# Optimization experiments

Measured on AMD Instinct MI355X. Metric: run time of the kernel, lower is better.

## Reference

```python
import jax, jax.numpy as jnp
import numpy as np

B, C, H, W = 8, 3, 1024, 1024
N, D, PS, NB, NH = 512, 256, 16, 8, 4


def _bin_matrix():
    # static radial-binning averaging matrix for a PS x (PS//2+1) rfft2 spectrum
    h, w = PS, PS // 2 + 1
    fy = np.fft.fftfreq(h)
    fx = np.linspace(0.0, 0.5, w)
    r = np.sqrt(fx[None, :] ** 2 + fy[:, None] ** 2)
    max_r = r.max() + 1e-6
    edges = np.linspace(0.0, max_r, NB + 1)
    idx = np.clip(np.searchsorted(edges, r.ravel(), side='right') - 1, 0, NB - 1)
    M = np.zeros((NB, h * w), np.float32)
    M[idx, np.arange(h * w)] = 1.0
    cnt = M.sum(1, keepdims=True)
    return M / np.maximum(cnt, 1.0)

_BIN_M = jnp.asarray(_bin_matrix())


def _ln(x, g, b, eps=1e-5):
    m = x.mean(-1, keepdims=True)
    v = x.var(-1, keepdims=True)
    return g * (x - m) / jnp.sqrt(v + eps) + b


def _gelu(x):
    return jax.nn.gelu(x, approximate=False)


def setup_inputs() -> dict:
    key = jax.random.key(0)
    ks = jax.random.split(key, 16)
    xav = lambda k, o, i: (jax.random.normal(k, (o, i)) / np.sqrt(i)).astype(jnp.float32)
    z = lambda n: jnp.zeros((n,), jnp.float32)
    o1 = lambda n: jnp.ones((n,), jnp.float32)
    FD = 2 * NB
    return {
        'image': jax.random.normal(ks[0], (B, C, H, W), jnp.float32),
        'point_coords': jax.random.uniform(ks[1], (B, N, 2), jnp.float32, 0.0, float(W)),
        'point_labels': jax.random.randint(ks[2], (B, N), 0, 2),
        'pe_w': xav(ks[3], D, D), 'pe_b': z(D),
        'type_emb': (0.02 * jax.random.normal(ks[4], (2, D))).astype(jnp.float32),
        'fbi': (1.0 + 0.1 * jax.random.normal(ks[5], (NB,))).astype(jnp.float32),
        'fe1_w': xav(ks[6], D // 2, FD), 'fe1_b': z(D // 2),
        'feln1_g': o1(D // 2), 'feln1_b': z(D // 2),
        'fe2_w': xav(ks[7], D, D // 2), 'fe2_b': z(D),
        'feln2_g': o1(D), 'feln2_b': z(D),
        'in_w': xav(ks[8], 3 * D, D), 'in_b': z(3 * D),
        'ao_w': xav(ks[9], D, D), 'ao_b': z(D),
        'n1_g': o1(D), 'n1_b': z(D),
        'f1_w': xav(ks[10], 2 * D, D), 'f1_b': z(2 * D),
        'f2_w': xav(ks[11], D, 2 * D), 'f2_b': z(D),
        'n2_g': o1(D), 'n2_b': z(D),
        'op_w': xav(ks[12], D, D), 'op_b': z(D),
    }


def reference(image, point_coords, point_labels, pe_w, pe_b, type_emb, fbi,
              fe1_w, fe1_b, feln1_g, feln1_b, fe2_w, fe2_b, feln2_g, feln2_b,
              in_w, in_b, ao_w, ao_b, n1_g, n1_b, f1_w, f1_b, f2_w, f2_b,
              n2_g, n2_b, op_w, op_b):
    Bv, Cv, Hv, Wv = image.shape
    Nv = point_coords.shape[1]
    # --- sinusoidal positional encoding (SAM style) + linear proj ---
    nc = point_coords / jnp.array([Wv, Hv], jnp.float32)
    dim_t = 10000.0 ** (2.0 * jnp.arange(D // 4, dtype=jnp.float32) / (D // 4))
    ax = (nc[..., 0:1] * (2.0 * np.pi)) / dim_t          # [B,N,D/4]
    ay = (nc[..., 1:2] * (2.0 * np.pi)) / dim_t
    pe = jnp.concatenate([jnp.sin(ax), jnp.cos(ax), jnp.sin(ay), jnp.cos(ay)], -1)
    spatial = pe @ pe_w.T + pe_b + type_emb[point_labels]  # [B,N,D]
    # --- batched per-point patch gather + rfft2 + radial binning ---
    gray = image.mean(1)                                   # [B,H,W]
    pc = jax.lax.stop_gradient(point_coords)               # .long() detaches in torch
    half = PS // 2
    px = jnp.clip(pc[..., 0].astype(jnp.int32), half, Wv - half - 1)
    py = jnp.clip(pc[..., 1].astype(jnp.int32), half, Hv - half - 1)
    off = jnp.arange(PS) - half
    rows = py[..., None] + off                             # [B,N,PS]
    cols = px[..., None] + off
    bidx = jnp.arange(Bv)[:, None, None, None]
    patches = gray[bidx, rows[..., :, None], cols[..., None, :]]  # [B,N,PS,PS]
    fft = jnp.fft.rfft2(patches, norm='ortho')             # [B,N,PS,PS//2+1]
    mag_bins = jnp.abs(fft).reshape(Bv, Nv, -1) @ _BIN_M.T    # [B,N,NB]
    ph_bins = jnp.angle(fft).reshape(Bv, Nv, -1) @ _BIN_M.T
    feat = jnp.concatenate([mag_bins * jax.nn.softmax(fbi), ph_bins], -1)  # [B,N,2*NB]
    # --- freq encoder MLP ---
    h1 = _gelu(_ln(feat @ fe1_w.T + fe1_b, feln1_g, feln1_b))
    freq = _ln(h1 @ fe2_w.T + fe2_b, feln2_g, feln2_b)     # [B,N,D]
    # --- cross-attention fusion (spatial = Q, freq = K/V) ---
    hd = D // NH
    q = (spatial @ in_w[:D].T + in_b[:D]).reshape(Bv, Nv, NH, hd)
    k = (freq @ in_w[D:2 * D].T + in_b[D:2 * D]).reshape(Bv, Nv, NH, hd)
    v = (freq @ in_w[2 * D:].T + in_b[2 * D:]).reshape(Bv, Nv, NH, hd)
    att = jax.nn.softmax(jnp.einsum('bqhd,bkhd->bhqk', q, k) / np.sqrt(hd), -1)
    o = jnp.einsum('bhqk,bkhd->bqhd', att, v).reshape(Bv, Nv, D)
    x = _ln(spatial + (o @ ao_w.T + ao_b), n1_g, n1_b)
    ffn = _gelu(x @ f1_w.T + f1_b) @ f2_w.T + f2_b
    x = _ln(x + ffn, n2_g, n2_b)
    return x @ op_w.T + op_b
```

## Files before the change

### kernel.cpp

```cpp
#include <hip/hip_runtime.h>
#include <math.h>


typedef __attribute__((ext_vector_type(8))) short short8;
typedef __attribute__((ext_vector_type(4))) float floatx4;
typedef unsigned short u16;
typedef unsigned long long u64;

__device__ __forceinline__ float gelu_f(float x) {
  return 0.5f * x * (1.0f + erff(x * 0.70710678118654752f));
}

__device__ __forceinline__ u16 bf16_rn(float x) {
  union { float f; unsigned u; } v; v.f = x;
  unsigned r = v.u + 0x7fffu + ((v.u >> 16) & 1u);
  return (u16)(r >> 16);
}

__device__ __forceinline__ void split_bf16(float x, u16& h, u16& l) {
  h = bf16_rn(x);
  union { unsigned u; float f; } hv; hv.u = ((unsigned)h) << 16;
  l = bf16_rn(x - hv.f);
}

#define W_PE   0
#define W_FE1  65536
#define W_FE2  67584
#define W_IN   100352
#define W_AO   296960
#define W_F1   362496
#define W_F2   493568
#define W_OP   624640


template <int NA, int K>
__device__ __forceinline__ void mm16_swz(
    const u16* Ah, const u16* Al, const int S,
    const u16* __restrict__ Bh, const u16* __restrict__ Bl,
    floatx4* acc)
{
  const int t = threadIdx.x;
  const int w = t >> 6, lane = t & 63;
  const int lm = lane & 15, kg = lane >> 4;
  #pragma unroll
  for (int it = 0; it < K / 32; ++it) {
    const short8 a_h = *(const short8*)&Ah[lm * S + it * 32 + kg * 8];
    const short8 a_l = *(const short8*)&Al[lm * S + it * 32 + kg * 8];
    #pragma unroll
    for (int nj = 0; nj < NA; nj++) {
      const size_t wo = (size_t)(((w * NA + nj) * (K / 32) + it) * 512 + lane * 8);
      const short8 b_h = *(const short8*)&Bh[wo];
      const short8 b_l = *(const short8*)&Bl[wo];
      acc[nj] = __builtin_amdgcn_mfma_f32_16x16x32_bf16(a_h, b_h, acc[nj], 0, 0, 0);
      acc[nj] = __builtin_amdgcn_mfma_f32_16x16x32_bf16(a_h, b_l, acc[nj], 0, 0, 0);
      acc[nj] = __builtin_amdgcn_mfma_f32_16x16x32_bf16(a_l, b_h, acc[nj], 0, 0, 0);
    }
  }
}

template <int NA, int K, int NSETS>
__device__ __forceinline__ void mm16_ks(
    const u16* Ah, const u16* Al, const int S,
    const u16* __restrict__ Bh, const u16* __restrict__ Bl,
    floatx4* acc)
{
  const int t = threadIdx.x;
  const int w = t >> 6, lane = t & 63;
  const int ww = w & 3, set = w >> 2;
  const int lm = lane & 15, kg = lane >> 4;
  constexpr int ITERS = K / (32 * NSETS);
  #pragma unroll
  for (int itl = 0; itl < ITERS; ++itl) {
    const int it = set * ITERS + itl;
    const short8 a_h = *(const short8*)&Ah[lm * S + it * 32 + kg * 8];
    const short8 a_l = *(const short8*)&Al[lm * S + it * 32 + kg * 8];
    #pragma unroll
    for (int nj = 0; nj < NA; nj++) {
      const size_t wo = (size_t)(((ww * NA + nj) * (K / 32) + it) * 512 + lane * 8);
      const short8 b_h = *(const short8*)&Bh[wo];
      const short8 b_l = *(const short8*)&Bl[wo];
      acc[nj] = __builtin_amdgcn_mfma_f32_16x16x32_bf16(a_h, b_h, acc[nj], 0, 0, 0);
      acc[nj] = __builtin_amdgcn_mfma_f32_16x16x32_bf16(a_h, b_l, acc[nj], 0, 0, 0);
      acc[nj] = __builtin_amdgcn_mfma_f32_16x16x32_bf16(a_l, b_h, acc[nj], 0, 0, 0);
    }
  }
}

template <int NA>
__device__ __forceinline__ void reduce_sets(floatx4* acc, float* PART)
{
  const int t = threadIdx.x;
  const int w = t >> 6, lane = t & 63;
  const int ww = w & 3, set = w >> 2;
  const int lm = lane & 15, kg = lane >> 4;
  __syncthreads();
  if (set != 0) {
    #pragma unroll
    for (int nj = 0; nj < NA; nj++) {
      const int col = ww * (NA * 16) + nj * 16 + lm;
      #pragma unroll
      for (int r = 0; r < 4; r++)
        PART[((set - 1) * 16 + kg * 4 + r) * 260 + col] = acc[nj][r];
    }
  }
  __syncthreads();
  if (set == 0) {
    #pragma unroll
    for (int nj = 0; nj < NA; nj++) {
      const int col = ww * (NA * 16) + nj * 16 + lm;
      #pragma unroll
      for (int r = 0; r < 4; r++) {
        const int rr = kg * 4 + r;
        acc[nj][r] += PART[rr * 260 + col] + PART[(16 + rr) * 260 + col]
                    + PART[(32 + rr) * 260 + col];
      }
    }
  }
}

template <int NA>
__device__ __forceinline__ void reduce_sets2(floatx4* acc, float* PART)
{
  const int t = threadIdx.x;
  const int w = t >> 6, lane = t & 63;
  const int ww = w & 3, set = w >> 2;
  const int lm = lane & 15, kg = lane >> 4;
  __syncthreads();
  if (set == 1) {
    #pragma unroll
    for (int nj = 0; nj < NA; nj++) {
      const int col = ww * (NA * 16) + nj * 16 + lm;
      #pragma unroll
      for (int r = 0; r < 4; r++)
        PART[(kg * 4 + r) * 260 + col] = acc[nj][r];
    }
  }
  __syncthreads();
  if (set == 0) {
    #pragma unroll
    for (int nj = 0; nj < NA; nj++) {
      const int col = ww * (NA * 16) + nj * 16 + lm;
      #pragma unroll
      for (int r = 0; r < 4; r++)
        acc[nj][r] += PART[(kg * 4 + r) * 260 + col];
    }
  }
}

__device__ __forceinline__ void stage16(
    const u16* __restrict__ Gh, const u16* __restrict__ Gl,
    u16* Lh, u16* Ll)
{
  const int t = threadIdx.x;
  #pragma unroll
  for (int i = 0; i < 2; i++) {
    const int s = t + i * 256;
    const int row = s >> 5, c = (s & 31) * 8;
    *(short8*)&Lh[row * 264 + c] = *(const short8*)&Gh[(size_t)row * 256 + c];
    *(short8*)&Ll[row * 264 + c] = *(const short8*)&Gl[(size_t)row * 256 + c];
  }
  __syncthreads();
}

template <int N_, int NA>
__device__ __forceinline__ void ln_rows(const float (&v)[NA][4], float* red1, float* red2,
                                        float (&mean)[4], float (&rstd)[4])
{
  const int t = threadIdx.x;
  const int w = t >> 6;
  const int lane = t & 63;
  const int kg = lane >> 4;
  float s1[4] = {0.f,0.f,0.f,0.f}, s2[4] = {0.f,0.f,0.f,0.f};
  #pragma unroll
  for (int nj = 0; nj < NA; nj++)
    #pragma unroll
    for (int r = 0; r < 4; r++) { s1[r] += v[nj][r]; s2[r] += v[nj][r] * v[nj][r]; }
  #pragma unroll
  for (int r = 0; r < 4; r++) {
    #pragma unroll
    for (int off = 1; off < 16; off <<= 1) {
      s1[r] += __shfl_xor(s1[r], off);
      s2[r] += __shfl_xor(s2[r], off);
    }
  }
  __syncthreads();
  if ((lane & 15) == 0) {
    #pragma unroll
    for (int r = 0; r < 4; r++) {
      red1[w * 16 + kg * 4 + r] = s1[r];
      red2[w * 16 + kg * 4 + r] = s2[r];
    }
  }
  __syncthreads();
  #pragma unroll
  for (int r = 0; r < 4; r++) {
    const int rw = kg * 4 + r;
    const float a = red1[rw] + red1[16 + rw] + red1[32 + rw] + red1[48 + rw];
    const float b = red2[rw] + red2[16 + rw] + red2[32 + rw] + red2[48 + rw];
    mean[r] = a * (1.0f / N_);
    rstd[r] = rsqrtf(b * (1.0f / N_) - mean[r] * mean[r] + 1e-5f);
  }
}

template <int N_, int NA>
__device__ __forceinline__ void ln_rows16(const float (&v)[NA][4], float* red1, float* red2,
                                          float (&mean)[4], float (&rstd)[4])
{
  const int t = threadIdx.x;
  const int w = t >> 6;
  const int lane = t & 63;
  const int ww = w & 3, set = w >> 2;
  const int kg = lane >> 4;
  float s1[4] = {0.f,0.f,0.f,0.f}, s2[4] = {0.f,0.f,0.f,0.f};
  #pragma unroll
  for (int nj = 0; nj < NA; nj++)
    #pragma unroll
    for (int r = 0; r < 4; r++) { s1[r] += v[nj][r]; s2[r] += v[nj][r] * v[nj][r]; }
  #pragma unroll
  for (int r = 0; r < 4; r++) {
    #pragma unroll
    for (int off = 1; off < 16; off <<= 1) {
      s1[r] += __shfl_xor(s1[r], off);
      s2[r] += __shfl_xor(s2[r], off);
    }
  }
  __syncthreads();
  if (set == 0 && (lane & 15) == 0) {
    #pragma unroll
    for (int r = 0; r < 4; r++) {
      red1[ww * 16 + kg * 4 + r] = s1[r];
      red2[ww * 16 + kg * 4 + r] = s2[r];
    }
  }
  __syncthreads();
  if (set == 0) {
    #pragma unroll
    for (int r = 0; r < 4; r++) {
      const int rw = kg * 4 + r;
      const float a = red1[rw] + red1[16 + rw] + red1[32 + rw] + red1[48 + rw];
      const float b = red2[rw] + red2[16 + rw] + red2[32 + rw] + red2[48 + rw];
      mean[r] = a * (1.0f / N_);
      rstd[r] = rsqrtf(b * (1.0f / N_) - mean[r] * mean[r] + 1e-5f);
    }
  }
}

__device__ __forceinline__ void store_swz(
    u16* __restrict__ Wh, u16* __restrict__ Wl, const int segbase,
    const int rel, const int kshift, const float4 v)
{
  const int K = 1 << kshift;
  const int n = rel >> kshift;
  const int k = rel & (K - 1);
  const int off8 = ((n >> 4) * (K >> 5) + (k >> 5)) * 512
                 + (((k >> 3) & 3) * 16 + (n & 15)) * 8 + (k & 7);
  u16 h0,h1,h2,h3,l0,l1,l2,l3;
  split_bf16(v.x,h0,l0); split_bf16(v.y,h1,l1);
  split_bf16(v.z,h2,l2); split_bf16(v.w,h3,l3);
  *(u64*)&Wh[segbase + off8] = (u64)h0 | ((u64)h1<<16) | ((u64)h2<<32) | ((u64)h3<<48);
  *(u64*)&Wl[segbase + off8] = (u64)l0 | ((u64)l1<<16) | ((u64)l2<<32) | ((u64)l3<<48);
}

__global__ __launch_bounds__(64) void k0_prep(
    const float* __restrict__ image, const float* __restrict__ coords,
    const float* __restrict__ fbi,
    const float* __restrict__ pe_w, const float* __restrict__ fe1_w,
    const float* __restrict__ fe2_w, const float* __restrict__ in_w,
    const float* __restrict__ ao_w, const float* __restrict__ f1_w,
    const float* __restrict__ f2_w, const float* __restrict__ op_w,
    u16* __restrict__ Wh, u16* __restrict__ Wl,
    u16* __restrict__ PEh, u16* __restrict__ PEl,
    u16* __restrict__ FEATh, u16* __restrict__ FEATl)
{
  const int blk = blockIdx.x;
  const int lane = threadIdx.x;

  if (blk < 2696) {
    const int idx = (blk * 64 + lane) * 4;
    if (idx < W_FE1) {
      store_swz(Wh, Wl, W_PE, idx - W_PE, 8, *(const float4*)&pe_w[idx - W_PE]);
    } else if (idx < W_FE2) {
      const int rel = idx - W_FE1;
      const float4 v = *(const float4*)&fe1_w[rel];
      u16 h0,h1,h2,h3,l0,l1,l2,l3;
      split_bf16(v.x,h0,l0); split_bf16(v.y,h1,l1);
      split_bf16(v.z,h2,l2); split_bf16(v.w,h3,l3);
      *(u64*)&Wh[idx] = (u64)h0 | ((u64)h1<<16) | ((u64)h2<<32) | ((u64)h3<<48);
      *(u64*)&Wl[idx] = (u64)l0 | ((u64)l1<<16) | ((u64)l2<<32) | ((u64)l3<<48);
    } else if (idx < W_IN) {
      store_swz(Wh, Wl, W_FE2, idx - W_FE2, 7, *(const float4*)&fe2_w[idx - W_FE2]);
    } else if (idx < W_AO) {
      store_swz(Wh, Wl, W_IN, idx - W_IN, 8, *(const float4*)&in_w[idx - W_IN]);
    } else if (idx < W_F1) {
      store_swz(Wh, Wl, W_AO, idx - W_AO, 8, *(const float4*)&ao_w[idx - W_AO]);
    } else if (idx < W_F2) {
      store_swz(Wh, Wl, W_F1, idx - W_F1, 8, *(const float4*)&f1_w[idx - W_F1]);
    } else if (idx < W_OP) {
      store_swz(Wh, Wl, W_F2, idx - W_F2, 9, *(const float4*)&f2_w[idx - W_F2]);
    } else {
      store_swz(Wh, Wl, W_OP, idx - W_OP, 8, *(const float4*)&op_w[idx - W_OP]);
    }
    return;
  }

  const int id = blk - 2696;
  const int b  = id >> 9;
  const float pcx = coords[id * 2 + 0];
  const float pcy = coords[id * 2 + 1];

  {
    const float TWO_PI = 6.283185307179586f;
    const float dimt = expf((float)lane * 0.28782313662425572f);
    const float ax = (pcx * (1.0f / 1024.0f)) * TWO_PI / dimt;
    const float ay = (pcy * (1.0f / 1024.0f)) * TWO_PI / dimt;
    u16 h, l;
    split_bf16(sinf(ax), h, l); PEh[id*256+lane]     = h; PEl[id*256+lane]     = l;
    split_bf16(cosf(ax), h, l); PEh[id*256+lane+64]  = h; PEl[id*256+lane+64]  = l;
    split_bf16(sinf(ay), h, l); PEh[id*256+lane+128] = h; PEl[id*256+lane+128] = l;
    split_bf16(cosf(ay), h, l); PEh[id*256+lane+192] = h; PEl[id*256+lane+192] = l;
  }

  int px = (int)pcx; px = px < 8 ? 8 : (px > 1015 ? 1015 : px);
  int py = (int)pcy; py = py < 8 ? 8 : (py > 1015 ? 1015 : py);

  __shared__ float patch[256];
  __shared__ float ct[16], st[16];
  __shared__ float Gre[144], Gim[144];
  __shared__ float msum[8], psum[8];
  __shared__ int cnt8[8];
  {
    const float* img = image + (size_t)b * 3145728;
    #pragma unroll
    for (int i = 0; i < 4; i++) {
      const int p = i * 64 + lane;
      const int r = p >> 4, c = p & 15;
      const int off = (py - 8 + r) * 1024 + (px - 8 + c);
      const float s = img[off] + img[off + 1048576] + img[off + 2097152];
      patch[r * 16 + c] = s * (1.0f / 3.0f);
    }
  }
  if (lane < 16) {
    float c, s;
    if ((lane & 3) == 0) {
      const float cv[4] = {1.0f, 0.0f, -1.0f, 0.0f};
      const float sv[4] = {0.0f, -1.0f, 0.0f, 1.0f};
      c = cv[lane >> 2]; s = sv[lane >> 2];
    } else {
      const float a = -3.14159265358979f * (float)lane * 0.125f;
      c = cosf(a); s = sinf(a);
    }
    ct[lane] = c; st[lane] = s;
  }
  if (lane < 8) { msum[lane] = 0.0f; psum[lane] = 0.0f; cnt8[lane] = 0; }
  __syncthreads();

  for (int tt = lane; tt < 144; tt += 64) {
    const int y = tt / 9, kx = tt - y * 9;
    float re = 0.0f, im = 0.0f;
    #pragma unroll
    for (int x = 0; x < 16; x++) {
      const int w = (x * kx) & 15;
      const float pv = patch[y * 16 + x];
      re = fmaf(pv, ct[w], re);
      im = fmaf(pv, st[w], im);
    }
    Gre[tt] = re; Gim[tt] = im;
  }
  __syncthreads();

  for (int tt = lane; tt < 144; tt += 64) {
    const int ky = tt / 9, kx = tt - ky * 9;
    float re = 0.0f, im = 0.0f;
    #pragma unroll
    for (int y = 0; y < 16; y++) {
      const int w = (y * ky) & 15;
      const float gr = Gre[y * 9 + kx], gi = Gim[y * 9 + kx];
      re = fmaf(gr, ct[w], re);
      re = fmaf(-gi, st[w], re);
      im = fmaf(gr, st[w], im);
      im = fmaf(gi, ct[w], im);
    }
    if (((ky & 7) == 0) && ((kx & 7) == 0)) im = 0.0f;
    const float mag = sqrtf(re * re + im * im) * 0.0625f;
    const float ph  = atan2f(im, re);

    const float fy = (ky < 8) ? (float)ky * 0.0625f : (float)(ky - 16) * 0.0625f;
    const float fx = (float)kx * 0.0625f;
    const float r = sqrtf(fx * fx + fy * fy);
    const float max_r = 0.7071077811865476f;
    const float stepf = max_r * 0.125f;
    int idx = 0;
    #pragma unroll
    for (int kq = 1; kq <= 8; kq++) {
      const float e = (kq == 8) ? max_r : stepf * (float)kq;
      if (r >= e) idx = kq;
    }
    if (idx > 7) idx = 7;
    atomicAdd(&msum[idx], mag);
    atomicAdd(&psum[idx], ph);
    atomicAdd(&cnt8[idx], 1);
  }
  __syncthreads();

  if (lane < 8) {
    float fm = fbi[0];
    #pragma unroll
    for (int j = 1; j < 8; j++) fm = fmaxf(fm, fbi[j]);
    float se = 0.0f;
    #pragma unroll
    for (int j = 0; j < 8; j++) se += expf(fbi[j] - fm);
    const float smx = expf(fbi[lane] - fm) / se;
    const float c = (float)(cnt8[lane] > 0 ? cnt8[lane] : 1);
    u16 h, l;
    split_bf16((msum[lane] / c) * smx, h, l);
    FEATh[id*16+lane] = h; FEATl[id*16+lane] = l;
    split_bf16(psum[lane] / c, h, l);
    FEATh[id*16+8+lane] = h; FEATl[id*16+8+lane] = l;
  }
}

__global__ __launch_bounds__(256) void k1_front(
    const u16* __restrict__ Wh, const u16* __restrict__ Wl,
    const u16* __restrict__ PEh, const u16* __restrict__ PEl,
    const u16* __restrict__ FEATh, const u16* __restrict__ FEATl,
    const float* __restrict__ pe_b, const int* __restrict__ labels,
    const float* __restrict__ temb,
    const float* __restrict__ fe1_b, const float* __restrict__ feln1_g, const float* __restrict__ feln1_b,
    const float* __restrict__ fe2_b, const float* __restrict__ feln2_g, const float* __restrict__ feln2_b,
    float* __restrict__ SPATIAL32, u16* __restrict__ SPh, u16* __restrict__ SPl,
    u16* __restrict__ FQh, u16* __restrict__ FQl)
{
  __shared__ __align__(16) u16 smem[8448];
  __shared__ float redbuf[128];
  const int blk = blockIdx.x;
  const int t = threadIdx.x;
  const int w = t >> 6, lane = t & 63;
  const int lm = lane & 15, kg = lane >> 4;

  if (blk < 256) {
    const int m0 = blk * 16;
    u16* Lh = smem;
    u16* Ll = smem + 4224;
    stage16(PEh + (size_t)m0 * 256, PEl + (size_t)m0 * 256, Lh, Ll);
    floatx4 acc[4];
    #pragma unroll
    for (int j = 0; j < 4; j++) acc[j] = (floatx4){0.f,0.f,0.f,0.f};
    mm16_swz<4, 256>(Lh, Ll, 264, Wh + W_PE, Wl + W_PE, acc);
    #pragma unroll
    for (int nj = 0; nj < 4; nj++) {
      const int col = w * 64 + nj * 16 + lm;
      #pragma unroll
      for (int r = 0; r < 4; r++) {
        const int row = m0 + kg * 4 + r;
        const float v = acc[nj][r] + pe_b[col] + temb[labels[row] * 256 + col];
        SPATIAL32[(size_t)row * 256 + col] = v;
        u16 h, l; split_bf16(v, h, l);
        SPh[(size_t)row * 256 + col] = h;
        SPl[(size_t)row * 256 + col] = l;
      }
    }
    return;
  }

  const int m0 = (blk - 256) * 16;
  u16* h1h = smem;
  u16* h1l = smem + 2176;

  floatx4 acc1[2];
  acc1[0] = (floatx4){0.f,0.f,0.f,0.f};
  acc1[1] = (floatx4){0.f,0.f,0.f,0.f};
  {
    const short8 zz = {0,0,0,0,0,0,0,0};
    const short8 a_h = (kg < 2) ? *(const short8*)&FEATh[(size_t)(m0 + lm) * 16 + kg * 8] : zz;
    const short8 a_l = (kg < 2) ? *(const short8*)&FEATl[(size_t)(m0 + lm) * 16 + kg * 8] : zz;
    #pragma unroll
    for (int nj = 0; nj < 2; nj++) {
      const int col = w * 32 + nj * 16 + lm;
      const short8 b_h = (kg < 2) ? *(const short8*)&Wh[W_FE1 + (size_t)col * 16 + kg * 8] : zz;
      const short8 b_l = (kg < 2) ? *(const short8*)&Wl[W_FE1 + (size_t)col * 16 + kg * 8] : zz;
      acc1[nj] = __builtin_amdgcn_mfma_f32_16x16x32_bf16(a_h, b_h, acc1[nj], 0, 0, 0);
      acc1[nj] = __builtin_amdgcn_mfma_f32_16x16x32_bf16(a_h, b_l, acc1[nj], 0, 0, 0);
      acc1[nj] = __builtin_amdgcn_mfma_f32_16x16x32_bf16(a_l, b_h, acc1[nj], 0, 0, 0);
    }
  }

  float v1[2][4];
  #pragma unroll
  for (int nj = 0; nj < 2; nj++) {
    const int col = w * 32 + nj * 16 + lm;
    #pragma unroll
    for (int r = 0; r < 4; r++) v1[nj][r] = acc1[nj][r] + fe1_b[col];
  }
  float mean[4], rstd[4];
  ln_rows<128, 2>(v1, redbuf, redbuf + 64, mean, rstd);
  #pragma unroll
  for (int nj = 0; nj < 2; nj++) {
    const int col = w * 32 + nj * 16 + lm;
    #pragma unroll
    for (int r = 0; r < 4; r++) {
      float y = feln1_g[col] * (v1[nj][r] - mean[r]) * rstd[r] + feln1_b[col];
      y = gelu_f(y);
      u16 h, l; split_bf16(y, h, l);
      h1h[(kg * 4 + r) * 136 + col] = h;
      h1l[(kg * 4 + r) * 136 + col] = l;
    }
  }
  __syncthreads();

  floatx4 acc2[4];
  #pragma unroll
  for (int j = 0; j < 4; j++) acc2[j] = (floatx4){0.f,0.f,0.f,0.f};
  mm16_swz<4, 128>(h1h, h1l, 136, Wh + W_FE2, Wl + W_FE2, acc2);

  float v2[4][4];
  #pragma unroll
  for (int nj = 0; nj < 4; nj++) {
    const int col = w * 64 + nj * 16 + lm;
    #pragma unroll
    for (int r = 0; r < 4; r++) v2[nj][r] = acc2[nj][r] + fe2_b[col];
  }
  ln_rows<256, 4>(v2, redbuf, redbuf + 64, mean, rstd);
  #pragma unroll
  for (int nj = 0; nj < 4; nj++) {
    const int col = w * 64 + nj * 16 + lm;
    #pragma unroll
    for (int r = 0; r < 4; r++) {
      const int rw = m0 + kg * 4 + r;
      float y = feln2_g[col] * (v2[nj][r] - mean[r]) * rstd[r] + feln2_b[col];
      u16 h, l; split_bf16(y, h, l);
      FQh[(size_t)rw * 256 + col] = h;
      FQl[(size_t)rw * 256 + col] = l;
    }
  }
}

__global__ __launch_bounds__(512) void k2_qkv(
    const u16* __restrict__ Wh, const u16* __restrict__ Wl,
    const u16* __restrict__ SPh, const u16* __restrict__ SPl,
    const u16* __restrict__ FQh, const u16* __restrict__ FQl,
    const float* __restrict__ in_b,
    u16* __restrict__ Qh, u16* __restrict__ Ql,
    u16* __restrict__ Kh, u16* __restrict__ Kl,
    u16* __restrict__ Vth, u16* __restrict__ Vtl)
{
  __shared__ __align__(16) u16 smem[8448];
  __shared__ float PART[16 * 260];
  const int bx = blockIdx.x;
  const int seg = bx >> 8;
  const int m0 = (bx & 255) * 16;
  const int t = threadIdx.x;
  const int w = t >> 6, lane = t & 63;
  const int ww = w & 3, set = w >> 2;
  const int lm = lane & 15, kg = lane >> 4;

  const u16 *Ah, *Al; const u16 *Wsh, *Wsl; const float* bias;
  if (seg == 0)      { Ah = SPh; Al = SPl; Wsh = Wh + W_IN;          Wsl = Wl + W_IN;          bias = in_b; }
  else if (seg == 1) { Ah = FQh; Al = FQl; Wsh = Wh + W_IN + 65536;  Wsl = Wl + W_IN + 65536;  bias = in_b + 256; }
  else               { Ah = FQh; Al = FQl; Wsh = Wh + W_IN + 131072; Wsl = Wl + W_IN + 131072; bias = in_b + 512; }

  u16* Lh = smem;
  u16* Ll = smem + 4224;
  {
    const u16* Gh = Ah + (size_t)m0 * 256;
    const u16* Gl = Al + (size_t)m0 * 256;
    const int row = t >> 5, c = (t & 31) * 8;
    *(short8*)&Lh[row * 264 + c] = *(const short8*)&Gh[(size_t)row * 256 + c];
    *(short8*)&Ll[row * 264 + c] = *(const short8*)&Gl[(size_t)row * 256 + c];
    __syncthreads();
  }

  floatx4 acc[4];
  #pragma unroll
  for (int j = 0; j < 4; j++) acc[j] = (floatx4){0.f,0.f,0.f,0.f};
  mm16_ks<4, 256, 2>(Lh, Ll, 264, Wsh, Wsl, acc);
  reduce_sets2<4>(acc, PART);

  if (set != 0) return;

  if (seg < 2) {
    u16* oh = (seg == 0) ? Qh : Kh;
    u16* ol = (seg == 0) ? Ql : Kl;
    #pragma unroll
    for (int nj = 0; nj < 4; nj++) {
      const int col = ww * 64 + nj * 16 + lm;
      #pragma unroll
      for (int r = 0; r < 4; r++) {
        const int row = m0 + kg * 4 + r;
        u16 h, l; split_bf16(acc[nj][r] + bias[col], h, l);
        oh[(size_t)row * 256 + col] = h;
        ol[(size_t)row * 256 + col] = l;
      }
    }
  } else {
    #pragma unroll
    for (int nj = 0; nj < 4; nj++) {
      const int col = ww * 64 + nj * 16 + lm;
      u64 hp = 0, lp = 0;
      #pragma unroll
      for (int r = 0; r < 4; r++) {
        u16 h, l; split_bf16(acc[nj][r] + bias[col], h, l);
        hp |= ((u64)h) << (16 * r);
        lp |= ((u64)l) << (16 * r);
      }
      *(u64*)&Vth[(size_t)col * 4096 + m0 + kg * 4] = hp;
      *(u64*)&Vtl[(size_t)col * 4096 + m0 + kg * 4] = lp;
    }
  }
}

__global__ __launch_bounds__(256) void k3_attn(
    const u16* __restrict__ Qh, const u16* __restrict__ Ql,
    const u16* __restrict__ Kh, const u16* __restrict__ Kl,
    const u16* __restrict__ Vth, const u16* __restrict__ Vtl,
    float* __restrict__ OP, float* __restrict__ ML)
{
  __shared__ __align__(16) u16 smem[36864];
  u16* sQh = smem;
  u16* sQl = smem + 4608;
  u16* sKh = smem + 9216;
  u16* sKl = smem + 13824;
  u16* sVh = smem + 18432;
  u16* sVl = smem + 23040;
  u16* sPh = smem + 27648;
  u16* sPl = smem + 32256;

  const int bx = blockIdx.x;
  const int half = bx & 1;
  const int qt = (bx >> 1) & 7;
  const int bh = bx >> 4;
  const int b = bh >> 2, h = bh & 3;
  const int t = threadIdx.x;
  const int w = t >> 6, lane = t & 63;
  const int lm = lane & 15, kg = lane >> 4;
  const int qrow0 = b * 512 + qt * 64;

  #pragma unroll
  for (int i = 0; i < 2; i++) {
    const int s = t + i * 256;
    const int r = s >> 3, d = (s & 7) * 8;
    *(short8*)&sQh[r * 72 + d] = *(const short8*)&Qh[(size_t)(qrow0 + r) * 256 + h * 64 + d];
    *(short8*)&sQl[r * 72 + d] = *(const short8*)&Ql[(size_t)(qrow0 + r) * 256 + h * 64 + d];
  }

  float m_i[4], l_i[4];
  floatx4 o_acc[4];
  #pragma unroll
  for (int r = 0; r < 4; r++) { m_i[r] = -INFINITY; l_i[r] = 0.0f; }
  #pragma unroll
  for (int dj = 0; dj < 4; dj++) o_acc[dj] = (floatx4){0.f, 0.f, 0.f, 0.f};

  __syncthreads();
  short8 q_h[2], q_l[2];
  #pragma unroll
  for (int ks = 0; ks < 2; ks++) {
    const int off = (w * 16 + lm) * 72 + ks * 32 + kg * 8;
    q_h[ks] = *(const short8*)&sQh[off];
    q_l[ks] = *(const short8*)&sQl[off];
  }

  for (int ktl = 0; ktl < 4; ktl++) {
    const int kt = half * 4 + ktl;
    __syncthreads();
    {
      const int krow0 = b * 512 + kt * 64;
      #pragma unroll
      for (int i = 0; i < 2; i++) {
        const int s = t + i * 256;
        const int r = s >> 3, d = (s & 7) * 8;
        *(short8*)&sKh[r * 72 + d] = *(const short8*)&Kh[(size_t)(krow0 + r) * 256 + h * 64 + d];
        *(short8*)&sKl[r * 72 + d] = *(const short8*)&Kl[(size_t)(krow0 + r) * 256 + h * 64 + d];
        *(short8*)&sVh[r * 72 + d] = *(const short8*)&Vth[(size_t)(h * 64 + r) * 4096 + krow0 + d];
        *(short8*)&sVl[r * 72 + d] = *(const short8*)&Vtl[(size_t)(h * 64 + r) * 4096 + krow0 + d];
      }
    }
    __syncthreads();

    floatx4 sacc[4];
    #pragma unroll
    for (int nj = 0; nj < 4; nj++) sacc[nj] = (floatx4){0.f, 0.f, 0.f, 0.f};
    #pragma unroll
    for (int ks = 0; ks < 2; ks++) {
      #pragma unroll
      for (int nj = 0; nj < 4; nj++) {
        const int off = (nj * 16 + lm) * 72 + ks * 32 + kg * 8;
        const short8 kb_h = *(const short8*)&sKh[off];
        const short8 kb_l = *(const short8*)&sKl[off];
        sacc[nj] = __builtin_amdgcn_mfma_f32_16x16x32_bf16(q_h[ks], kb_h, sacc[nj], 0, 0, 0);
        sacc[nj] = __builtin_amdgcn_mfma_f32_16x16x32_bf16(q_h[ks], kb_l, sacc[nj], 0, 0, 0);
        sacc[nj] = __builtin_amdgcn_mfma_f32_16x16x32_bf16(q_l[ks], kb_h, sacc[nj], 0, 0, 0);
      }
    }

    float pp[4][4];
    #pragma unroll
    for (int r = 0; r < 4; r++) {
      float mx = -INFINITY;
      #pragma unroll
      for (int nj = 0; nj < 4; nj++) {
        sacc[nj][r] *= 0.125f;
        mx = fmaxf(mx, sacc[nj][r]);
      }
      #pragma unroll
      for (int off = 1; off < 16; off <<= 1) mx = fmaxf(mx, __shfl_xor(mx, off));
      const float mnew = fmaxf(m_i[r], mx);
      const float alpha = expf(m_i[r] - mnew);
      m_i[r] = mnew;
      float rs = 0.0f;
      #pragma unroll
      for (int nj = 0; nj < 4; nj++) { pp[nj][r] = expf(sacc[nj][r] - mnew); rs += pp[nj][r]; }
      #pragma unroll
      for (int off = 1; off < 16; off <<= 1) rs += __shfl_xor(rs, off);
      l_i[r] = l_i[r] * alpha + rs;
      #pragma unroll
      for (int dj = 0; dj < 4; dj++) o_acc[dj][r] *= alpha;
    }

    #pragma unroll
    for (int nj = 0; nj < 4; nj++)
      #pragma unroll
      for (int r = 0; r < 4; r++) {
        u16 ph, pl; split_bf16(pp[nj][r], ph, pl);
        sPh[(w * 16 + kg * 4 + r) * 72 + nj * 16 + lm] = ph;
        sPl[(w * 16 + kg * 4 + r) * 72 + nj * 16 + lm] = pl;
      }

    #pragma unroll
    for (int ks = 0; ks < 2; ks++) {
      const short8 p_h = *(const short8*)&sPh[(w * 16 + lm) * 72 + ks * 32 + kg * 8];
      const short8 p_l = *(const short8*)&sPl[(w * 16 + lm) * 72 + ks * 32 + kg * 8];
      #pragma unroll
      for (int dj = 0; dj < 4; dj++) {
        const int off = (dj * 16 + lm) * 72 + ks * 32 + kg * 8;
        const short8 v_h = *(const short8*)&sVh[off];
        const short8 v_l = *(const short8*)&sVl[off];
        o_acc[dj] = __builtin_amdgcn_mfma_f32_16x16x32_bf16(p_h, v_h, o_acc[dj], 0, 0, 0);
        o_acc[dj] = __builtin_amdgcn_mfma_f32_16x16x32_bf16(p_l, v_h, o_acc[dj], 0, 0, 0);
        o_acc[dj] = __builtin_amdgcn_mfma_f32_16x16x32_bf16(p_h, v_l, o_acc[dj], 0, 0, 0);
      }
    }
  }

  #pragma unroll
  for (int r = 0; r < 4; r++) {
    const int row = w * 16 + kg * 4 + r;
    const int grow = qrow0 + row;
    if (lm == 0) {
      ML[half * 32768 + grow * 8 + h * 2]     = m_i[r];
      ML[half * 32768 + grow * 8 + h * 2 + 1] = l_i[r];
    }
    #pragma unroll
    for (int dj = 0; dj < 4; dj++)
      OP[(size_t)half * 1048576 + (size_t)grow * 256 + h * 64 + dj * 16 + lm] = o_acc[dj][r];
  }
}

__global__ __launch_bounds__(256) void k3_merge(
    const float* __restrict__ OP, const float* __restrict__ ML,
    u16* __restrict__ Oh, u16* __restrict__ Ol)
{
  const int tid = blockIdx.x * 256 + threadIdx.x;
  const int row = tid >> 6;
  const int c4 = (tid & 63) * 4;
  const int h = c4 >> 6;
  const float m0v = ML[row * 8 + h * 2],         l0v = ML[row * 8 + h * 2 + 1];
  const float m1v = ML[32768 + row * 8 + h * 2], l1v = ML[32768 + row * 8 + h * 2 + 1];
  const float mn = fmaxf(m0v, m1v);
  const float a0 = expf(m0v - mn), a1 = expf(m1v - mn);
  const float inv = 1.0f / (l0v * a0 + l1v * a1);
  const float4 v0 = *(const float4*)&OP[(size_t)row * 256 + c4];
  const float4 v1 = *(const float4*)&OP[1048576 + (size_t)row * 256 + c4];
  const float mv[4] = {
    (v0.x * a0 + v1.x * a1) * inv, (v0.y * a0 + v1.y * a1) * inv,
    (v0.z * a0 + v1.z * a1) * inv, (v0.w * a0 + v1.w * a1) * inv };
  u64 hp = 0, lp = 0;
  #pragma unroll
  for (int i = 0; i < 4; i++) {
    u16 hx, lx; split_bf16(mv[i], hx, lx);
    hp |= ((u64)hx) << (16 * i);
    lp |= ((u64)lx) << (16 * i);
  }
  *(u64*)&Oh[(size_t)row * 256 + c4] = hp;
  *(u64*)&Ol[(size_t)row * 256 + c4] = lp;
}

__global__ __launch_bounds__(1024) void k4_tail(
    const u16* __restrict__ Wh, const u16* __restrict__ Wl,
    const u16* __restrict__ Oh, const u16* __restrict__ Ol,
    const float* __restrict__ SPATIAL32,
    const float* __restrict__ ao_b, const float* __restrict__ n1_g, const float* __restrict__ n1_b,
    const float* __restrict__ f1_b, const float* __restrict__ f2_b,
    const float* __restrict__ n2_g, const float* __restrict__ n2_b,
    const float* __restrict__ op_b, float* __restrict__ OUT)
{
  __shared__ __align__(16) u16 smem[25088];
  __shared__ float redbuf[128];
  __shared__ float PART[3 * 16 * 260];
  u16* B1h = smem;
  u16* B1l = smem + 4224;
  u16* Fh  = smem + 8448;
  u16* Fl  = smem + 16768;

  const int t = threadIdx.x;
  const int w = t >> 6, lane = t & 63;
  const int ww = w & 3, set = w >> 2;
  const int lm = lane & 15, kg = lane >> 4;
  const int m0 = blockIdx.x * 16;

  {
    const u16* Gh = Oh + (size_t)m0 * 256;
    const u16* Gl = Ol + (size_t)m0 * 256;
    if (t < 512) {
      const int row = t >> 5, c = (t & 31) * 8;
      *(short8*)&B1h[row * 264 + c] = *(const short8*)&Gh[(size_t)row * 256 + c];
      *(short8*)&B1l[row * 264 + c] = *(const short8*)&Gl[(size_t)row * 256 + c];
    }
    __syncthreads();
  }

  floatx4 acc[4];
  #pragma unroll
  for (int j = 0; j < 4; j++) acc[j] = (floatx4){0.f,0.f,0.f,0.f};
  mm16_ks<4, 256, 4>(B1h, B1l, 264, Wh + W_AO, Wl + W_AO, acc);
  reduce_sets<4>(acc, PART);

  float x1reg[4][4];
  {
    float v[4][4];
    if (set == 0) {
      #pragma unroll
      for (int nj = 0; nj < 4; nj++) {
        const int col = ww * 64 + nj * 16 + lm;
        #pragma unroll
        for (int r = 0; r < 4; r++)
          v[nj][r] = acc[nj][r] + ao_b[col] + SPATIAL32[(size_t)(m0 + kg * 4 + r) * 256 + col];
      }
    } else {
      #pragma unroll
      for (int nj = 0; nj < 4; nj++)
        #pragma unroll
        for (int r = 0; r < 4; r++) v[nj][r] = 0.0f;
    }
    float mean[4], rstd[4];
    ln_rows16<256, 4>(v, redbuf, redbuf + 64, mean, rstd);
    if (set == 0) {
      #pragma unroll
      for (int nj = 0; nj < 4; nj++) {
        const int col = ww * 64 + nj * 16 + lm;
        #pragma unroll
        for (int r = 0; r < 4; r++) {
          const float y = n1_g[col] * (v[nj][r] - mean[r]) * rstd[r] + n1_b[col];
          x1reg[nj][r] = y;
          u16 h, l; split_bf16(y, h, l);
          B1h[(kg * 4 + r) * 264 + col] = h;
          B1l[(kg * 4 + r) * 264 + col] = l;
        }
      }
    }
  }
  __syncthreads();

  #pragma unroll
  for (int ct = 0; ct < 2; ct++) {
    floatx4 a4[4];
    #pragma unroll
    for (int j = 0; j < 4; j++) a4[j] = (floatx4){0.f,0.f,0.f,0.f};
    mm16_ks<4, 256, 4>(B1h, B1l, 264,
                       Wh + W_F1 + (size_t)ct * 65536, Wl + W_F1 + (size_t)ct * 65536, a4);
    reduce_sets<4>(a4, PART);
    if (set == 0) {
      #pragma unroll
      for (int nj = 0; nj < 4; nj++) {
        const int col = ct * 256 + ww * 64 + nj * 16 + lm;
        #pragma unroll
        for (int r = 0; r < 4; r++) {
          const float y = gelu_f(a4[nj][r] + f1_b[col]);
          u16 h, l; split_bf16(y, h, l);
          Fh[(kg * 4 + r) * 520 + col] = h;
          Fl[(kg * 4 + r) * 520 + col] = l;
        }
      }
    }
  }
  __syncthreads();

  #pragma unroll
  for (int j = 0; j < 4; j++) acc[j] = (floatx4){0.f,0.f,0.f,0.f};
  mm16_ks<4, 512, 4>(Fh, Fl, 520, Wh + W_F2, Wl + W_F2, acc);
  reduce_sets<4>(acc, PART);
  {
    float v[4][4];
    if (set == 0) {
      #pragma unroll
      for (int nj = 0; nj < 4; nj++) {
        const int col = ww * 64 + nj * 16 + lm;
        #pragma unroll
        for (int r = 0; r < 4; r++)
          v[nj][r] = acc[nj][r] + f2_b[col] + x1reg[nj][r];
      }
    } else {
      #pragma unroll
      for (int nj = 0; nj < 4; nj++)
        #pragma unroll
        for (int r = 0; r < 4; r++) v[nj][r] = 0.0f;
    }
    float mean[4], rstd[4];
    ln_rows16<256, 4>(v, redbuf, redbuf + 64, mean, rstd);
    if (set == 0) {
      #pragma unroll
      for (int nj = 0; nj < 4; nj++) {
        const int col = ww * 64 + nj * 16 + lm;
        #pragma unroll
        for (int r = 0; r < 4; r++) {
          const float y = n2_g[col] * (v[nj][r] - mean[r]) * rstd[r] + n2_b[col];
          u16 h, l; split_bf16(y, h, l);
          B1h[(kg * 4 + r) * 264 + col] = h;
          B1l[(kg * 4 + r) * 264 + col] = l;
        }
      }
    }
  }
  __syncthreads();

  #pragma unroll
  for (int j = 0; j < 4; j++) acc[j] = (floatx4){0.f,0.f,0.f,0.f};
  mm16_ks<4, 256, 4>(B1h, B1l, 264, Wh + W_OP, Wl + W_OP, acc);
  reduce_sets<4>(acc, PART);
  if (set == 0) {
    #pragma unroll
    for (int nj = 0; nj < 4; nj++) {
      const int col = ww * 64 + nj * 16 + lm;
      #pragma unroll
      for (int r = 0; r < 4; r++)
        OUT[(size_t)(m0 + kg * 4 + r) * 256 + col] = acc[nj][r] + op_b[col];
    }
  }
}

extern "C" void kernel_launch(void* const* d_in, const int* in_sizes, int n_in,
                              void* d_out, int out_size, void* d_ws, size_t ws_size,
                              hipStream_t stream) {
  const float* image   = (const float*)d_in[0];
  const float* coords  = (const float*)d_in[1];
  const int*   labels  = (const int*)d_in[2];
  const float* pe_w    = (const float*)d_in[3];
  const float* pe_b    = (const float*)d_in[4];
  const float* temb    = (const float*)d_in[5];
  const float* fbi     = (const float*)d_in[6];
  const float* fe1_w   = (const float*)d_in[7];
  const float* fe1_b   = (const float*)d_in[8];
  const float* feln1_g = (const float*)d_in[9];
  const float* feln1_b = (const float*)d_in[10];
  const float* fe2_w   = (const float*)d_in[11];
  const float* fe2_b   = (const float*)d_in[12];
  const float* feln2_g = (const float*)d_in[13];
  const float* feln2_b = (const float*)d_in[14];
  const float* in_w    = (const float*)d_in[15];
  const float* in_b    = (const float*)d_in[16];
  const float* ao_w    = (const float*)d_in[17];
  const float* ao_b    = (const float*)d_in[18];
  const float* n1_g    = (const float*)d_in[19];
  const float* n1_b    = (const float*)d_in[20];
  const float* f1_w    = (const float*)d_in[21];
  const float* f1_b    = (const float*)d_in[22];
  const float* f2_w    = (const float*)d_in[23];
  const float* f2_b    = (const float*)d_in[24];
  const float* n2_g    = (const float*)d_in[25];
  const float* n2_b    = (const float*)d_in[26];
  const float* op_w    = (const float*)d_in[27];
  const float* op_b    = (const float*)d_in[28];

  float* ws = (float*)d_ws;
  float* SPATIAL32 = ws;
  u16* S = (u16*)(ws + 2 * (1u << 20));
  u16* Wh = S;
  u16* Wl = S + 690176;
  u16* PEh   = S + 1380352;  u16* PEl   = PEh + 1048576;
  u16* FEATh = S + 3477504;  u16* FEATl = FEATh + 65536;
  u16* FQh   = S + 4657152;  u16* FQl   = FQh + 1048576;
  u16* SPh   = S + 6754304;  u16* SPl   = SPh + 1048576;
  u16* Qh    = S + 8851456;  u16* Ql    = Qh + 1048576;
  u16* Kh    = S + 10948608; u16* Kl    = Kh + 1048576;
  u16* Vth   = S + 13045760; u16* Vtl   = Vth + 1048576;
  float* OP  = (float*)(S + 15142912);
  float* ML  = (float*)(S + 19337216);
  u16* Oh    = S + 19468288; u16* Ol = Oh + 1048576;

  float* OUT = (float*)d_out;

  k0_prep<<<6792, 64, 0, stream>>>(
      image, coords, fbi, pe_w, fe1_w, fe2_w, in_w, ao_w, f1_w, f2_w, op_w,
      Wh, Wl, PEh, PEl, FEATh, FEATl);
  k1_front<<<512, 256, 0, stream>>>(
      Wh, Wl, PEh, PEl, FEATh, FEATl, pe_b, labels, temb,
      fe1_b, feln1_g, feln1_b, fe2_b, feln2_g, feln2_b,
      SPATIAL32, SPh, SPl, FQh, FQl);
  k2_qkv<<<768, 512, 0, stream>>>(
      Wh, Wl, SPh, SPl, FQh, FQl, in_b, Qh, Ql, Kh, Kl, Vth, Vtl);
  k3_attn<<<512, 256, 0, stream>>>(Qh, Ql, Kh, Kl, Vth, Vtl, OP, ML);
  k3_merge<<<1024, 256, 0, stream>>>(OP, ML, Oh, Ol);
  k4_tail<<<256, 1024, 0, stream>>>(
      Wh, Wl, Oh, Ol, SPATIAL32, ao_b, n1_g, n1_b, f1_b, f2_b, n2_g, n2_b, op_b, OUT);
}
```

Measured before the change: 287.0 us.

## Split attention over all eight key tiles and read K/V directly from global

The attention kernel now launches one block per (batch, head, query tile, key tile), giving 2048 blocks instead of 512 with a two-way key split and a four-tile loop. Each block computes a single-tile softmax and writes partial outputs plus max and sum. The merge kernel then combines eight partials instead of two. K and V are loaded straight from global memory into MFMA operands rather than staged through shared memory, which removes the staging barriers and cuts LDS use. In exchange, partial-output traffic grows fourfold (8 float buffers of 4 MB each), and the workspace offsets for ML and Oh are moved to make room.

Result: slower. 332.9 us (+16.0%).

```diff
diff --git a/kernel.cpp b/kernel.cpp
--- a/kernel.cpp
+++ b/kernel.cpp
@@ -614,129 +614,88 @@
     const u16* __restrict__ Vth, const u16* __restrict__ Vtl,
     float* __restrict__ OP, float* __restrict__ ML)
 {
-  __shared__ __align__(16) u16 smem[36864];
-  u16* sQh = smem;
-  u16* sQl = smem + 4608;
-  u16* sKh = smem + 9216;
-  u16* sKl = smem + 13824;
-  u16* sVh = smem + 18432;
-  u16* sVl = smem + 23040;
-  u16* sPh = smem + 27648;
-  u16* sPl = smem + 32256;
+  __shared__ __align__(16) u16 sPh[4608];
+  __shared__ __align__(16) u16 sPl[4608];
 
   const int bx = blockIdx.x;
-  const int half = bx & 1;
-  const int qt = (bx >> 1) & 7;
-  const int bh = bx >> 4;
+  const int kt = bx & 7;
+  const int qt = (bx >> 3) & 7;
+  const int bh = bx >> 6;
   const int b = bh >> 2, h = bh & 3;
   const int t = threadIdx.x;
   const int w = t >> 6, lane = t & 63;
   const int lm = lane & 15, kg = lane >> 4;
   const int qrow0 = b * 512 + qt * 64;
-
-  #pragma unroll
-  for (int i = 0; i < 2; i++) {
-    const int s = t + i * 256;
-    const int r = s >> 3, d = (s & 7) * 8;
-    *(short8*)&sQh[r * 72 + d] = *(const short8*)&Qh[(size_t)(qrow0 + r) * 256 + h * 64 + d];
-    *(short8*)&sQl[r * 72 + d] = *(const short8*)&Ql[(size_t)(qrow0 + r) * 256 + h * 64 + d];
-  }
-
-  float m_i[4], l_i[4];
+  const int krow0 = b * 512 + kt * 64;
+
+  short8 q_h[2], q_l[2];
+  #pragma unroll
+  for (int ks = 0; ks < 2; ks++) {
+    const size_t qo = (size_t)(qrow0 + w * 16 + lm) * 256 + h * 64 + ks * 32 + kg * 8;
+    q_h[ks] = *(const short8*)&Qh[qo];
+    q_l[ks] = *(const short8*)&Ql[qo];
+  }
+
+  floatx4 sacc[4];
+  #pragma unroll
+  for (int nj = 0; nj < 4; nj++) sacc[nj] = (floatx4){0.f, 0.f, 0.f, 0.f};
+  #pragma unroll
+  for (int ks = 0; ks < 2; ks++) {
+    #pragma unroll
+    for (int nj = 0; nj < 4; nj++) {
+      const size_t ko = (size_t)(krow0 + nj * 16 + lm) * 256 + h * 64 + ks * 32 + kg * 8;
+      const short8 kb_h = *(const short8*)&Kh[ko];
+      const short8 kb_l = *(const short8*)&Kl[ko];
+      sacc[nj] = __builtin_amdgcn_mfma_f32_16x16x32_bf16(q_h[ks], kb_h, sacc[nj], 0, 0, 0);
+      sacc[nj] = __builtin_amdgcn_mfma_f32_16x16x32_bf16(q_h[ks], kb_l, sacc[nj], 0, 0, 0);
+      sacc[nj] = __builtin_amdgcn_mfma_f32_16x16x32_bf16(q_l[ks], kb_h, sacc[nj], 0, 0, 0);
+    }
+  }
+
+  float m_i[4], l_i[4], pp[4][4];
+  #pragma unroll
+  for (int r = 0; r < 4; r++) {
+    float mx = -INFINITY;
+    #pragma unroll
+    for (int nj = 0; nj < 4; nj++) {
+      sacc[nj][r] *= 0.125f;
+      mx = fmaxf(mx, sacc[nj][r]);
+    }
+    #pragma unroll
+    for (int off = 1; off < 16; off <<= 1) mx = fmaxf(mx, __shfl_xor(mx, off));
+    m_i[r] = mx;
+    float rs = 0.0f;
+    #pragma unroll
+    for (int nj = 0; nj < 4; nj++) { pp[nj][r] = expf(sacc[nj][r] - mx); rs += pp[nj][r]; }
+    #pragma unroll
+    for (int off = 1; off < 16; off <<= 1) rs += __shfl_xor(rs, off);
+    l_i[r] = rs;
+  }
+
+  #pragma unroll
+  for (int nj = 0; nj < 4; nj++)
+    #pragma unroll
+    for (int r = 0; r < 4; r++) {
+      u16 ph, pl; split_bf16(pp[nj][r], ph, pl);
+      sPh[(w * 16 + kg * 4 + r) * 72 + nj * 16 + lm] = ph;
+      sPl[(w * 16 + kg * 4 + r) * 72 + nj * 16 + lm] = pl;
+    }
+
   floatx4 o_acc[4];
   #pragma unroll
-  for (int r = 0; r < 4; r++) { m_i[r] = -INFINITY; l_i[r] = 0.0f; }
-  #pragma unroll
   for (int dj = 0; dj < 4; dj++) o_acc[dj] = (floatx4){0.f, 0.f, 0.f, 0.f};
-
-  __syncthreads();
-  short8 q_h[2], q_l[2];
   #pragma unroll
   for (int ks = 0; ks < 2; ks++) {
-    const int off = (w * 16 + lm) * 72 + ks * 32 + kg * 8;
-    q_h[ks] = *(const short8*)&sQh[off];
-    q_l[ks] = *(const short8*)&sQl[off];
-  }
-
-  for (int ktl = 0; ktl < 4; ktl++) {
-    const int kt = half * 4 + ktl;
-    __syncthreads();
-    {
-      const int krow0 = b * 512 + kt * 64;
-      #pragma unroll
-      for (int i = 0; i < 2; i++) {
-        const int s = t + i * 256;
-        const int r = s >> 3, d = (s & 7) * 8;
-        *(short8*)&sKh[r * 72 + d] = *(const short8*)&Kh[(size_t)(krow0 + r) * 256 + h * 64 + d];
-        *(short8*)&sKl[r * 72 + d] = *(const short8*)&Kl[(size_t)(krow0 + r) * 256 + h * 64 + d];
-        *(short8*)&sVh[r * 72 + d] = *(const short8*)&Vth[(size_t)(h * 64 + r) * 4096 + krow0 + d];
-        *(short8*)&sVl[r * 72 + d] = *(const short8*)&Vtl[(size_t)(h * 64 + r) * 4096 + krow0 + d];
-      }
-    }
-    __syncthreads();
-
-    floatx4 sacc[4];
-    #pragma unroll
-    for (int nj = 0; nj < 4; nj++) sacc[nj] = (floatx4){0.f, 0.f, 0.f, 0.f};
-    #pragma unroll
-    for (int ks = 0; ks < 2; ks++) {
-      #pragma unroll
-      for (int nj = 0; nj < 4; nj++) {
-        const int off = (nj * 16 + lm) * 72 + ks * 32 + kg * 8;
-        const short8 kb_h = *(const short8*)&sKh[off];
-        const short8 kb_l = *(const short8*)&sKl[off];
-        sacc[nj] = __builtin_amdgcn_mfma_f32_16x16x32_bf16(q_h[ks], kb_h, sacc[nj], 0, 0, 0);
-        sacc[nj] = __builtin_amdgcn_mfma_f32_16x16x32_bf16(q_h[ks], kb_l, sacc[nj], 0, 0, 0);
-        sacc[nj] = __builtin_amdgcn_mfma_f32_16x16x32_bf16(q_l[ks], kb_h, sacc[nj], 0, 0, 0);
-      }
-    }
-
-    float pp[4][4];
-    #pragma unroll
-    for (int r = 0; r < 4; r++) {
-      float mx = -INFINITY;
-      #pragma unroll
-      for (int nj = 0; nj < 4; nj++) {
-        sacc[nj][r] *= 0.125f;
-        mx = fmaxf(mx, sacc[nj][r]);
-      }
-      #pragma unroll
-      for (int off = 1; off < 16; off <<= 1) mx = fmaxf(mx, __shfl_xor(mx, off));
-      const float mnew = fmaxf(m_i[r], mx);
-      const float alpha = expf(m_i[r] - mnew);
-      m_i[r] = mnew;
-      float rs = 0.0f;
-      #pragma unroll
-      for (int nj = 0; nj < 4; nj++) { pp[nj][r] = expf(sacc[nj][r] - mnew); rs += pp[nj][r]; }
-      #pragma unroll
-      for (int off = 1; off < 16; off <<= 1) rs += __shfl_xor(rs, off);
-      l_i[r] = l_i[r] * alpha + rs;
-      #pragma unroll
-      for (int dj = 0; dj < 4; dj++) o_acc[dj][r] *= alpha;
-    }
-
-    #pragma unroll
-    for (int nj = 0; nj < 4; nj++)
-      #pragma unroll
-      for (int r = 0; r < 4; r++) {
-        u16 ph, pl; split_bf16(pp[nj][r], ph, pl);
-        sPh[(w * 16 + kg * 4 + r) * 72 + nj * 16 + lm] = ph;
-        sPl[(w * 16 + kg * 4 + r) * 72 + nj * 16 + lm] = pl;
-      }
-
-    #pragma unroll
-    for (int ks = 0; ks < 2; ks++) {
-      const short8 p_h = *(const short8*)&sPh[(w * 16 + lm) * 72 + ks * 32 + kg * 8];
-      const short8 p_l = *(const short8*)&sPl[(w * 16 + lm) * 72 + ks * 32 + kg * 8];
-      #pragma unroll
-      for (int dj = 0; dj < 4; dj++) {
-        const int off = (dj * 16 + lm) * 72 + ks * 32 + kg * 8;
-        const short8 v_h = *(const short8*)&sVh[off];
-        const short8 v_l = *(const short8*)&sVl[off];
-        o_acc[dj] = __builtin_amdgcn_mfma_f32_16x16x32_bf16(p_h, v_h, o_acc[dj], 0, 0, 0);
-        o_acc[dj] = __builtin_amdgcn_mfma_f32_16x16x32_bf16(p_l, v_h, o_acc[dj], 0, 0, 0);
-        o_acc[dj] = __builtin_amdgcn_mfma_f32_16x16x32_bf16(p_h, v_l, o_acc[dj], 0, 0, 0);
-      }
+    const short8 p_h = *(const short8*)&sPh[(w * 16 + lm) * 72 + ks * 32 + kg * 8];
+    const short8 p_l = *(const short8*)&sPl[(w * 16 + lm) * 72 + ks * 32 + kg * 8];
+    #pragma unroll
+    for (int dj = 0; dj < 4; dj++) {
+      const size_t vo = (size_t)(h * 64 + dj * 16 + lm) * 4096 + krow0 + ks * 32 + kg * 8;
+      const short8 v_h = *(const short8*)&Vth[vo];
+      const short8 v_l = *(const short8*)&Vtl[vo];
+      o_acc[dj] = __builtin_amdgcn_mfma_f32_16x16x32_bf16(p_h, v_h, o_acc[dj], 0, 0, 0);
+      o_acc[dj] = __builtin_amdgcn_mfma_f32_16x16x32_bf16(p_l, v_h, o_acc[dj], 0, 0, 0);
+      o_acc[dj] = __builtin_amdgcn_mfma_f32_16x16x32_bf16(p_h, v_l, o_acc[dj], 0, 0, 0);
     }
   }
 
@@ -745,12 +704,12 @@
     const int row = w * 16 + kg * 4 + r;
     const int grow = qrow0 + row;
     if (lm == 0) {
-      ML[half * 32768 + grow * 8 + h * 2]     = m_i[r];
-      ML[half * 32768 + grow * 8 + h * 2 + 1] = l_i[r];
+      ML[kt * 32768 + grow * 8 + h * 2]     = m_i[r];
+      ML[kt * 32768 + grow * 8 + h * 2 + 1] = l_i[r];
     }
     #pragma unroll
     for (int dj = 0; dj < 4; dj++)
-      OP[(size_t)half * 1048576 + (size_t)grow * 256 + h * 64 + dj * 16 + lm] = o_acc[dj][r];
+      OP[(size_t)kt * 1048576 + (size_t)grow * 256 + h * 64 + dj * 16 + lm] = o_acc[dj][r];
   }
 }
 
@@ -762,16 +721,27 @@
   const int row = tid >> 6;
   const int c4 = (tid & 63) * 4;
   const int h = c4 >> 6;
-  const float m0v = ML[row * 8 + h * 2],         l0v = ML[row * 8 + h * 2 + 1];
-  const float m1v = ML[32768 + row * 8 + h * 2], l1v = ML[32768 + row * 8 + h * 2 + 1];
-  const float mn = fmaxf(m0v, m1v);
-  const float a0 = expf(m0v - mn), a1 = expf(m1v - mn);
-  const float inv = 1.0f / (l0v * a0 + l1v * a1);
-  const float4 v0 = *(const float4*)&OP[(size_t)row * 256 + c4];
-  const float4 v1 = *(const float4*)&OP[1048576 + (size_t)row * 256 + c4];
-  const float mv[4] = {
-    (v0.x * a0 + v1.x * a1) * inv, (v0.y * a0 + v1.y * a1) * inv,
-    (v0.z * a0 + v1.z * a1) * inv, (v0.w * a0 + v1.w * a1) * inv };
+  float m[8], l[8];
+  float mn = -INFINITY;
+  #pragma unroll
+  for (int i = 0; i < 8; i++) {
+    m[i] = ML[i * 32768 + row * 8 + h * 2];
+    l[i] = ML[i * 32768 + row * 8 + h * 2 + 1];
+    mn = fmaxf(mn, m[i]);
+  }
+  float a[8];
+  float denom = 0.0f;
+  #pragma unroll
+  for (int i = 0; i < 8; i++) { a[i] = expf(m[i] - mn); denom += l[i] * a[i]; }
+  const float inv = 1.0f / denom;
+  float4 acc = {0.f, 0.f, 0.f, 0.f};
+  #pragma unroll
+  for (int i = 0; i < 8; i++) {
+    const float4 v = *(const float4*)&OP[(size_t)i * 1048576 + (size_t)row * 256 + c4];
+    acc.x += v.x * a[i]; acc.y += v.y * a[i];
+    acc.z += v.z * a[i]; acc.w += v.w * a[i];
+  }
+  const float mv[4] = { acc.x * inv, acc.y * inv, acc.z * inv, acc.w * inv };
   u64 hp = 0, lp = 0;
   #pragma unroll
   for (int i = 0; i < 4; i++) {
@@ -982,8 +952,8 @@
   u16* Kh    = S + 10948608; u16* Kl    = Kh + 1048576;
   u16* Vth   = S + 13045760; u16* Vtl   = Vth + 1048576;
   float* OP  = (float*)(S + 15142912);
-  float* ML  = (float*)(S + 19337216);
-  u16* Oh    = S + 19468288; u16* Ol = Oh + 1048576;
+  float* ML  = (float*)(S + 31920128);
+  u16* Oh    = S + 32444416; u16* Ol = Oh + 1048576;
 
   float* OUT = (float*)d_out;
 
@@ -996,7 +966,7 @@
       SPATIAL32, SPh, SPl, FQh, FQl);
   k2_qkv<<<768, 512, 0, stream>>>(
       Wh, Wl, SPh, SPl, FQh, FQl, in_b, Qh, Ql, Kh, Kl, Vth, Vtl);
-  k3_attn<<<512, 256, 0, stream>>>(Qh, Ql, Kh, Kl, Vth, Vtl, OP, ML);
+  k3_attn<<<2048, 256, 0, stream>>>(Qh, Ql, Kh, Kl, Vth, Vtl, OP, ML);
   k3_merge<<<1024, 256, 0, stream>>>(OP, ML, Oh, Ol);
   k4_tail<<<256, 1024, 0, stream>>>(
       Wh, Wl, Oh, Ol, SPATIAL32, ao_b, n1_g, n1_b, f1_b, f2_b, n2_g, n2_b, op_b, OUT);
```
